# Performance work log

Measured on AMD Instinct MI355X. Metric: run time of the kernel, lower is better.

Reference implementation:

```python
import jax, jax.numpy as jnp
import numpy as np

B, T, H, W = 2, 32, 16, 16
D, NH = 256, 8
DH = D // NH


def _block_causal(Tn, block):
    # True = allowed to attend (block-lower-triangular over time blocks)
    base = jnp.triu(jnp.ones((Tn, Tn), bool), 1)
    return ~jnp.repeat(jnp.repeat(base, block, 0), block, 1)


def _ln(x, g, b, eps=1e-5):
    mu = x.mean(-1, keepdims=True)
    var = ((x - mu) ** 2).mean(-1, keepdims=True)
    return (x - mu) * jax.lax.rsqrt(var + eps) * g + b


def _attn(q, k, v, mask=None):
    # q,k,v: [Bf, S, h, dh]
    s = jnp.einsum('bqhd,bkhd->bhqk', q, k) * (q.shape[-1] ** -0.5)
    if mask is not None:
        s = jnp.where(mask, s, jnp.finfo(s.dtype).min)
    a = jax.nn.softmax(s, -1)
    return jnp.einsum('bhqk,bkhd->bqhd', a, v)


def setup_inputs() -> dict:
    key = jax.random.key(0)
    ks = iter(jax.random.split(key, 64))

    def lin(din, dout):
        return (jax.random.normal(next(ks), (din, dout), jnp.float32) * 0.02,
                jnp.zeros((dout,), jnp.float32))

    inp = {'x': jax.random.normal(next(ks), (B, T, H, W, D), jnp.float32)}
    inp['g1'] = jnp.ones((D,), jnp.float32); inp['b1'] = jnp.zeros((D,), jnp.float32)
    for plane in ('hw', 'ht', 'wt'):
        for p in ('q', 'k', 'v'):
            w, b = lin(D, D)
            inp[f'w{p}_{plane}'] = w
            inp[f'b{p}_{plane}'] = b
    inp['wo'], inp['bo'] = lin(D, D)
    inp['wg1'], inp['bg1'] = lin(D, D)
    inp['wg2'], inp['bg2'] = lin(D, 3 * NH)
    inp['g2'] = jnp.ones((D,), jnp.float32); inp['b2'] = jnp.zeros((D,), jnp.float32)
    inp['wm1'], inp['bm1'] = lin(D, 4 * D)
    inp['wm2'], inp['bm2'] = lin(4 * D, D)
    return inp


def reference(x, g1, b1,
              wq_hw, bq_hw, wk_hw, bk_hw, wv_hw, bv_hw,
              wq_ht, bq_ht, wk_ht, bk_ht, wv_ht, bv_ht,
              wq_wt, bq_wt, wk_wt, bk_wt, wv_wt, bv_wt,
              wo, bo, wg1, bg1, wg2, bg2, g2, b2,
              wm1, bm1, wm2, bm2):
    y = _ln(x, g1, b1)

    # HW plane: attention over H*W at each (B,T), non-causal
    def hw(w, b):
        return (y @ w + b).reshape(B * T, H * W, NH, DH)
    o_hw = _attn(hw(wq_hw, bq_hw), hw(wk_hw, bk_hw), hw(wv_hw, bv_hw))
    o_hw = o_hw.reshape(B, T, H, W, NH, DH)

    # HT plane: fixed W column, seq = T*H, block-causal in T (block H)
    def ht(w, b):
        return (y @ w + b).reshape(B, T, H, W, NH, DH).transpose(0, 3, 1, 2, 4, 5).reshape(B * W, T * H, NH, DH)
    mask_ht = _block_causal(T, H)[None, None]
    o_ht = _attn(ht(wq_ht, bq_ht), ht(wk_ht, bk_ht), ht(wv_ht, bv_ht), mask_ht)
    o_ht = o_ht.reshape(B, W, T, H, NH, DH).transpose(0, 2, 3, 1, 4, 5)

    # WT plane: fixed H row, seq = T*W, block-causal in T (block W)
    def wt(w, b):
        return (y @ w + b).reshape(B, T, H, W, NH, DH).transpose(0, 2, 1, 3, 4, 5).reshape(B * H, T * W, NH, DH)
    mask_wt = _block_causal(T, W)[None, None]
    o_wt = _attn(wt(wq_wt, bq_wt), wt(wk_wt, bk_wt), wt(wv_wt, bv_wt), mask_wt)
    o_wt = o_wt.reshape(B, H, T, W, NH, DH).transpose(0, 2, 1, 3, 4, 5)

    # per-head gated fusion across the three planes
    gates = jax.nn.softmax((jax.nn.silu(y @ wg1 + bg1) @ wg2 + bg2).reshape(B, T, H, W, NH, 3), -1)
    m = gates[..., 0:1] * o_hw + gates[..., 1:2] * o_ht + gates[..., 2:3] * o_wt

    x = x + m.reshape(B, T, H, W, D) @ wo + bo
    x = x + (jax.nn.gelu(_ln(x, g2, b2) @ wm1 + bm1, approximate=False) @ wm2 + bm2)
    return x
```

## Files before the change

### kernel.cpp

```cpp
#include <hip/hip_runtime.h>
#include <math.h>

#define NTOK 16384
#define DD   256
#define NHD  8
#define DHD  32

typedef unsigned short ushort_t;
using short8  = __attribute__((ext_vector_type(8))) short;
using floatx4 = __attribute__((ext_vector_type(4))) float;

__device__ __forceinline__ ushort_t f2bf(float f) {
  unsigned u = __float_as_uint(f);
  u = (u + 0x7FFFu + ((u >> 16) & 1u)) >> 16;
  return (ushort_t)u;
}

__device__ __forceinline__ float wave_sum(float v) {
#pragma unroll
  for (int off = 32; off; off >>= 1) v += __shfl_xor(v, off, 64);
  return v;
}

__global__ __launch_bounds__(256) void ln_bf_kernel(
    const float* __restrict__ x, const float* __restrict__ g,
    const float* __restrict__ b, ushort_t* __restrict__ y)
{
  const int row  = blockIdx.x * 4 + (threadIdx.x >> 6);
  const int lane = threadIdx.x & 63;
  const float4 xv = *(const float4*)&x[(size_t)row * DD + lane * 4];
  float s = xv.x + xv.y + xv.z + xv.w;
  s = wave_sum(s);
  const float mu = s * (1.0f / DD);
  const float dx = xv.x - mu, dy = xv.y - mu, dz = xv.z - mu, dw = xv.w - mu;
  float ss = dx * dx + dy * dy + dz * dz + dw * dw;
  ss = wave_sum(ss);
  const float rs = rsqrtf(ss * (1.0f / DD) + 1e-5f);
  const float4 gv = *(const float4*)&g[lane * 4];
  const float4 bv = *(const float4*)&b[lane * 4];
  ushort4 o;
  o.x = f2bf(dx * rs * gv.x + bv.x);
  o.y = f2bf(dy * rs * gv.y + bv.y);
  o.z = f2bf(dz * rs * gv.z + bv.z);
  o.w = f2bf(dw * rs * gv.w + bv.w);
  *(ushort4*)&y[(size_t)row * DD + lane * 4] = o;
}

struct W11 { const float* s[11]; ushort_t* d[11]; };

__global__ __launch_bounds__(256) void convw11_kernel(W11 p) {
  const int mi = blockIdx.y;
  const int idx = blockIdx.x * 256 + threadIdx.x;
  const int n = idx >> 8, k = idx & 255;
  p.d[mi][n * 256 + k] = f2bf(p.s[mi][k * 256 + n]);
}

template <int KK, int NN>
__global__ __launch_bounds__(256) void convw_kernel(
    const float* __restrict__ src, ushort_t* __restrict__ dst)
{
  const int idx = blockIdx.x * 256 + threadIdx.x;
  const int n = idx / KK, k = idx % KK;
  dst[n * KK + k] = f2bf(src[(size_t)k * NN + n]);
}

#define LDK 40

template <bool RES>
__device__ __forceinline__ void mgemm_body(
    const ushort_t* __restrict__ A, const ushort_t* __restrict__ Wt,
    const float* __restrict__ bias, const float* __restrict__ res,
    void* __restrict__ Cout, int M, int N, int K, int bx, int by,
    int act, bool obf)
{
  __shared__ ushort_t As[128 * LDK];
  __shared__ ushort_t Bs[128 * LDK];
  const int tid = threadIdx.x;
  const int wid = tid >> 6;
  const int lane = tid & 63;
  const int wm = (wid >> 1) * 64;
  const int wn = (wid & 1) * 64;
  const int m0 = by * 128, n0 = bx * 128;

  const int lrow = tid >> 1;
  const int lk   = (tid & 1) * 16;
  const int fr = lane & 15;
  const int fk = (lane >> 4) * 8;

  floatx4 acc[4][4] = {};

  uint4 av0 = *(const uint4*)&A[(size_t)(m0 + lrow) * K + lk];
  uint4 av1 = *(const uint4*)&A[(size_t)(m0 + lrow) * K + lk + 8];
  uint4 bv0 = *(const uint4*)&Wt[(size_t)(n0 + lrow) * K + lk];
  uint4 bv1 = *(const uint4*)&Wt[(size_t)(n0 + lrow) * K + lk + 8];

  for (int k0 = 0; k0 < K; k0 += 32) {
    __syncthreads();
    *(uint4*)&As[lrow * LDK + lk]     = av0;
    *(uint4*)&As[lrow * LDK + lk + 8] = av1;
    *(uint4*)&Bs[lrow * LDK + lk]     = bv0;
    *(uint4*)&Bs[lrow * LDK + lk + 8] = bv1;
    __syncthreads();
    if (k0 + 32 < K) {
      av0 = *(const uint4*)&A[(size_t)(m0 + lrow) * K + k0 + 32 + lk];
      av1 = *(const uint4*)&A[(size_t)(m0 + lrow) * K + k0 + 32 + lk + 8];
      bv0 = *(const uint4*)&Wt[(size_t)(n0 + lrow) * K + k0 + 32 + lk];
      bv1 = *(const uint4*)&Wt[(size_t)(n0 + lrow) * K + k0 + 32 + lk + 8];
    }
    short8 af[4], bf[4];
#pragma unroll
    for (int f = 0; f < 4; f++) {
      af[f] = *(const short8*)&As[(wm + f * 16 + fr) * LDK + fk];
      bf[f] = *(const short8*)&Bs[(wn + f * 16 + fr) * LDK + fk];
    }
#pragma unroll
    for (int i = 0; i < 4; i++)
#pragma unroll
      for (int j = 0; j < 4; j++)
        acc[i][j] = __builtin_amdgcn_mfma_f32_16x16x32_bf16(af[i], bf[j], acc[i][j], 0, 0, 0);
  }

  const int g4 = (lane >> 4) * 4;
#pragma unroll
  for (int i = 0; i < 4; i++) {
#pragma unroll
    for (int j = 0; j < 4; j++) {
      const int col = n0 + wn + j * 16 + fr;
      const float bb = bias[col];
#pragma unroll
      for (int r = 0; r < 4; r++) {
        const int row = m0 + wm + i * 16 + g4 + r;
        float v = acc[i][j][r] + bb;
        if (act == 1) v = v / (1.0f + __expf(-v));
        if (act == 2) v = 0.5f * v * (1.0f + erff(v * 0.70710678118654752f));
        if (RES) v += res[(size_t)row * N + col];
        if (obf) ((ushort_t*)Cout)[(size_t)row * N + col] = f2bf(v);
        else     ((float*)Cout)[(size_t)row * N + col] = v;
      }
    }
  }
}

template <int ACT, bool RES, bool OBF>
__global__ __launch_bounds__(256) void mgemm_kernel(
    const ushort_t* __restrict__ A, const ushort_t* __restrict__ Wt,
    const float* __restrict__ bias, const float* __restrict__ res,
    void* __restrict__ C, int M, int N, int K)
{
  mgemm_body<RES>(A, Wt, bias, res, C, M, N, K, blockIdx.x, blockIdx.y, ACT, OBF);
}

struct ProjArgs {
  const ushort_t* w[10];
  const float*    b[10];
  void*           c[10];
};

__global__ __launch_bounds__(256) void mgemm_proj_kernel(
    const ushort_t* __restrict__ A, ProjArgs p, int M, int N, int K)
{
  const int z = blockIdx.z;
  const int act = (z == 9) ? 1 : 0;
  const bool obf = (z != 9);
  mgemm_body<false>(A, p.w[z], p.b[z], nullptr, p.c[z], M, N, K,
                    blockIdx.x, blockIdx.y, act, obf);
}

template <bool RES>
__global__ __launch_bounds__(256) void mgemm64_kernel(
    const ushort_t* __restrict__ A, const ushort_t* __restrict__ Wt,
    const float* __restrict__ bias, const float* __restrict__ res,
    float* __restrict__ C, int M, int N, int K)
{
  __shared__ ushort_t As[64 * LDK];
  __shared__ ushort_t Bs[64 * LDK];
  const int tid = threadIdx.x;
  const int wid = tid >> 6;
  const int lane = tid & 63;
  const int wm = (wid >> 1) * 32;
  const int wn = (wid & 1) * 32;
  const int m0 = blockIdx.y * 64, n0 = blockIdx.x * 64;

  const int lr = tid >> 2;
  const int lq = (tid & 3) * 8;
  const int fr = lane & 15;
  const int fk = (lane >> 4) * 8;

  floatx4 acc[2][2] = {};

  uint4 av = *(const uint4*)&A[(size_t)(m0 + lr) * K + lq];
  uint4 bv = *(const uint4*)&Wt[(size_t)(n0 + lr) * K + lq];

  for (int k0 = 0; k0 < K; k0 += 32) {
    __syncthreads();
    *(uint4*)&As[lr * LDK + lq] = av;
    *(uint4*)&Bs[lr * LDK + lq] = bv;
    __syncthreads();
    if (k0 + 32 < K) {
      av = *(const uint4*)&A[(size_t)(m0 + lr) * K + k0 + 32 + lq];
      bv = *(const uint4*)&Wt[(size_t)(n0 + lr) * K + k0 + 32 + lq];
    }
    short8 af[2], bf[2];
#pragma unroll
    for (int f = 0; f < 2; f++) {
      af[f] = *(const short8*)&As[(wm + f * 16 + fr) * LDK + fk];
      bf[f] = *(const short8*)&Bs[(wn + f * 16 + fr) * LDK + fk];
    }
#pragma unroll
    for (int i = 0; i < 2; i++)
#pragma unroll
      for (int j = 0; j < 2; j++)
        acc[i][j] = __builtin_amdgcn_mfma_f32_16x16x32_bf16(af[i], bf[j], acc[i][j], 0, 0, 0);
  }

  const int g4 = (lane >> 4) * 4;
#pragma unroll
  for (int i = 0; i < 2; i++) {
#pragma unroll
    for (int j = 0; j < 2; j++) {
      const int col = n0 + wn + j * 16 + fr;
      const float bb = bias[col];
#pragma unroll
      for (int r = 0; r < 4; r++) {
        const int row = m0 + wm + i * 16 + g4 + r;
        float v = acc[i][j][r] + bb;
        if (RES) v += res[(size_t)row * N + col];
        C[(size_t)row * N + col] = v;
      }
    }
  }
}

__device__ __forceinline__ int tok_map_rt(int plane, int bb, int s) {
  if (plane == 0) return bb * 256 + s;
  if (plane == 1) return (bb >> 4) * 8192 + (s >> 4) * 256 + (s & 15) * 16 + (bb & 15);
  return (bb >> 4) * 8192 + (s >> 4) * 256 + (bb & 15) * 16 + (s & 15);
}

__global__ __launch_bounds__(256) void mattn_all_kernel(
    const ushort_t* __restrict__ qkv, float* __restrict__ ohw,
    float* __restrict__ oht, float* __restrict__ owt)
{
  __shared__ ushort_t Kls[64 * 40];
  __shared__ ushort_t Vt[32 * 72];
  __shared__ ushort_t Pls[4 * 16 * 72];

  const int head = blockIdx.x;
  const int yy = blockIdx.y;
  const int plane = yy >> 8;
  const int rm = yy & 255;
  int qc, bb, S;
  bool causal;
  if (plane == 0) { qc = rm >> 6; bb = rm & 63; S = 256; causal = false; }
  else            { qc = rm >> 5; bb = rm & 31; S = 512; causal = true;  }

  const size_t NDU = (size_t)NTOK * DD;
  const ushort_t* Qg = qkv + (size_t)(plane * 3 + 0) * NDU;
  const ushort_t* Kg = qkv + (size_t)(plane * 3 + 1) * NDU;
  const ushort_t* Vg = qkv + (size_t)(plane * 3 + 2) * NDU;
  float* Og = (plane == 0) ? ohw : (plane == 1) ? oht : owt;

  const int tid = threadIdx.x;
  const int wid = tid >> 6;
  const int lane = tid & 63;
  const int fr = lane & 15;
  const int hi = lane >> 4;
  const float scale = 0.17677669529663687f;

  const int q0 = qc * 64;

  const int qtok_a = tok_map_rt(plane, bb, q0 + wid * 16 + fr);
  const short8 qfrag = *(const short8*)&Qg[(size_t)qtok_a * DD + head * DHD + hi * 8];

  floatx4 o0 = {}, o1 = {};
  float mrun[4] = {-3e30f, -3e30f, -3e30f, -3e30f};
  float lrun[4] = {0.f, 0.f, 0.f, 0.f};

  const int lim = causal ? (q0 + wid * 16 + 16) : S;
  const int ntiles = (causal ? (q0 + 64) : S) >> 6;

  const int krow = tid >> 2;
  const int g    = tid & 3;
  const int kseg = g * 8;

  int ptok = tok_map_rt(plane, bb, krow);
  uint4 kv = *(const uint4*)&Kg[(size_t)ptok * DD + head * DHD + kseg];
  uint4 vv = *(const uint4*)&Vg[(size_t)ptok * DD + head * DHD + kseg];

  for (int t = 0; t < ntiles; t++) {
    __syncthreads();
    *(uint4*)&Kls[krow * 40 + kseg] = kv;
    {
      const ushort_t* vp = (const ushort_t*)&vv;
#pragma unroll
      for (int d = 0; d < 8; d++) {
        const int dim = kseg + d;
        Vt[dim * 72 + (((krow >> 3) ^ (dim >> 2)) << 3) + (krow & 7)] = vp[d];
      }
    }
    __syncthreads();
    if (t + 1 < ntiles) {
      ptok = tok_map_rt(plane, bb, (t + 1) * 64 + krow);
      kv = *(const uint4*)&Kg[(size_t)ptok * DD + head * DHD + kseg];
      vv = *(const uint4*)&Vg[(size_t)ptok * DD + head * DHD + kseg];
    }

    const int kt0 = t * 64;
    if (causal && kt0 >= lim) continue;
    const int kend = causal ? min(lim - kt0, 64) : 64;

    floatx4 sacc[4];
#pragma unroll
    for (int j = 0; j < 4; j++) {
      floatx4 z = {};
      const short8 kf = *(const short8*)&Kls[(j * 16 + fr) * 40 + hi * 8];
      sacc[j] = __builtin_amdgcn_mfma_f32_16x16x32_bf16(qfrag, kf, z, 0, 0, 0);
    }

    float sc[4][4];
    float mt[4] = {-3e30f, -3e30f, -3e30f, -3e30f};
#pragma unroll
    for (int j = 0; j < 4; j++) {
      const bool valid = !causal || (j * 16 + fr) < kend;
#pragma unroll
      for (int r = 0; r < 4; r++) {
        const float sv = valid ? sacc[j][r] * scale : -3e30f;
        sc[j][r] = sv;
        mt[r] = fmaxf(mt[r], sv);
      }
    }
#pragma unroll
    for (int r = 0; r < 4; r++) {
      mt[r] = fmaxf(mt[r], __shfl_xor(mt[r], 1, 64));
      mt[r] = fmaxf(mt[r], __shfl_xor(mt[r], 2, 64));
      mt[r] = fmaxf(mt[r], __shfl_xor(mt[r], 4, 64));
      mt[r] = fmaxf(mt[r], __shfl_xor(mt[r], 8, 64));
    }

    float corr[4], psum[4];
#pragma unroll
    for (int r = 0; r < 4; r++) {
      const float mnew = fmaxf(mrun[r], mt[r]);
      corr[r] = __expf(mrun[r] - mnew);
      mrun[r] = mnew;
      psum[r] = 0.f;
    }

    const int pbase = wid * (16 * 72);
#pragma unroll
    for (int j = 0; j < 4; j++) {
#pragma unroll
      for (int r = 0; r < 4; r++) {
        const float p = __expf(sc[j][r] - mrun[r]);
        const ushort_t pb = f2bf(p);
        psum[r] += __uint_as_float((unsigned)pb << 16);
        Pls[pbase + (hi * 4 + r) * 72 + (((2 * j + (fr >> 3)) ^ hi) << 3) + (fr & 7)] = pb;
      }
    }
#pragma unroll
    for (int r = 0; r < 4; r++) {
      psum[r] += __shfl_xor(psum[r], 1, 64);
      psum[r] += __shfl_xor(psum[r], 2, 64);
      psum[r] += __shfl_xor(psum[r], 4, 64);
      psum[r] += __shfl_xor(psum[r], 8, 64);
      lrun[r] = lrun[r] * corr[r] + psum[r];
      o0[r] *= corr[r];
      o1[r] *= corr[r];
    }

#pragma unroll
    for (int kh = 0; kh < 2; kh++) {
      const int bq = (hi + 4 * kh);
      const short8 pa  = *(const short8*)&Pls[pbase + fr * 72 + ((bq ^ (fr >> 2)) << 3)];
      const short8 vb0 = *(const short8*)&Vt[fr * 72 + ((bq ^ (fr >> 2)) << 3)];
      const short8 vb1 = *(const short8*)&Vt[(16 + fr) * 72 + ((bq ^ ((fr >> 2) + 4)) << 3)];
      o0 = __builtin_amdgcn_mfma_f32_16x16x32_bf16(pa, vb0, o0, 0, 0, 0);
      o1 = __builtin_amdgcn_mfma_f32_16x16x32_bf16(pa, vb1, o1, 0, 0, 0);
    }
  }

#pragma unroll
  for (int r = 0; r < 4; r++) {
    const float inv = 1.0f / lrun[r];
    const int otok = tok_map_rt(plane, bb, q0 + wid * 16 + hi * 4 + r);
    float* ob = &Og[(size_t)otok * DD + head * DHD];
    ob[fr] = o0[r] * inv;
    ob[16 + fr] = o1[r] * inv;
  }
}

__global__ __launch_bounds__(256) void gate_kernel(
    const float* __restrict__ t, const float* __restrict__ wg2,
    const float* __restrict__ bg2, float* __restrict__ gates)
{
  const int idx = blockIdx.x * 256 + threadIdx.x;
  const int token = idx >> 3, head = idx & 7;
  float a0 = bg2[head * 3 + 0], a1 = bg2[head * 3 + 1], a2 = bg2[head * 3 + 2];
  const float* trow = &t[(size_t)token * DD];
  const float* wbase = &wg2[head * 3];
  for (int k4 = 0; k4 < 64; k4++) {
    const float4 tv = *(const float4*)&trow[k4 * 4];
    const float* wr = &wbase[(k4 * 4) * 24];
    a0 = fmaf(tv.x, wr[0],      a0); a1 = fmaf(tv.x, wr[1],      a1); a2 = fmaf(tv.x, wr[2],      a2);
    a0 = fmaf(tv.y, wr[24 + 0], a0); a1 = fmaf(tv.y, wr[24 + 1], a1); a2 = fmaf(tv.y, wr[24 + 2], a2);
    a0 = fmaf(tv.z, wr[48 + 0], a0); a1 = fmaf(tv.z, wr[48 + 1], a1); a2 = fmaf(tv.z, wr[48 + 2], a2);
    a0 = fmaf(tv.w, wr[72 + 0], a0); a1 = fmaf(tv.w, wr[72 + 1], a1); a2 = fmaf(tv.w, wr[72 + 2], a2);
  }
  const float mx = fmaxf(a0, fmaxf(a1, a2));
  const float e0 = __expf(a0 - mx), e1 = __expf(a1 - mx), e2 = __expf(a2 - mx);
  const float inv = 1.0f / (e0 + e1 + e2);
  float* gp = &gates[(size_t)token * 24 + head * 3];
  gp[0] = e0 * inv; gp[1] = e1 * inv; gp[2] = e2 * inv;
}

__global__ __launch_bounds__(256) void combine_kernel(
    const float* __restrict__ gates, const float* __restrict__ ohw,
    const float* __restrict__ oht, const float* __restrict__ owt,
    ushort_t* __restrict__ m)
{
  const int idx = blockIdx.x * 256 + threadIdx.x;
  const int token = idx >> 6;
  const int head = (idx >> 3) & 7;
  const float* gp = &gates[(size_t)token * 24 + head * 3];
  const float g0 = gp[0], g1 = gp[1], g2 = gp[2];
  const float4 a = ((const float4*)ohw)[idx];
  const float4 b = ((const float4*)oht)[idx];
  const float4 c = ((const float4*)owt)[idx];
  ushort4 r;
  r.x = f2bf(g0 * a.x + g1 * b.x + g2 * c.x);
  r.y = f2bf(g0 * a.y + g1 * b.y + g2 * c.y);
  r.z = f2bf(g0 * a.z + g1 * b.z + g2 * c.z);
  r.w = f2bf(g0 * a.w + g1 * b.w + g2 * c.w);
  ((ushort4*)m)[idx] = r;
}

extern "C" void kernel_launch(void* const* d_in, const int* in_sizes, int n_in,
                              void* d_out, int out_size, void* d_ws, size_t ws_size,
                              hipStream_t stream)
{
  (void)in_sizes; (void)n_in; (void)out_size; (void)ws_size;
  const float* x   = (const float*)d_in[0];
  const float* g1  = (const float*)d_in[1];
  const float* b1  = (const float*)d_in[2];
  const float* wq[3] = {(const float*)d_in[3], (const float*)d_in[9],  (const float*)d_in[15]};
  const float* bq[3] = {(const float*)d_in[4], (const float*)d_in[10], (const float*)d_in[16]};
  const float* wk[3] = {(const float*)d_in[5], (const float*)d_in[11], (const float*)d_in[17]};
  const float* bk[3] = {(const float*)d_in[6], (const float*)d_in[12], (const float*)d_in[18]};
  const float* wv[3] = {(const float*)d_in[7], (const float*)d_in[13], (const float*)d_in[19]};
  const float* bv[3] = {(const float*)d_in[8], (const float*)d_in[14], (const float*)d_in[20]};
  const float* wo  = (const float*)d_in[21];
  const float* bo  = (const float*)d_in[22];
  const float* wg1 = (const float*)d_in[23];
  const float* bg1 = (const float*)d_in[24];
  const float* wg2 = (const float*)d_in[25];
  const float* bg2 = (const float*)d_in[26];
  const float* g2  = (const float*)d_in[27];
  const float* b2  = (const float*)d_in[28];
  const float* wm1 = (const float*)d_in[29];
  const float* bm1 = (const float*)d_in[30];
  const float* wm2 = (const float*)d_in[31];
  const float* bm2 = (const float*)d_in[32];

  const size_t NDU = (size_t)NTOK * DD;

  ushort_t* U = (ushort_t*)d_ws;
  ushort_t* Ybf  = U;
  ushort_t* Y2bf = U + NDU;
  ushort_t* qkvb = U + 2 * NDU;
  ushort_t* Mbf  = U + 11 * NDU;
  float* F   = (float*)(U + 12 * NDU);
  float* Ohw = F;
  float* Oht = Ohw + NDU;
  float* Owt = Oht + NDU;
  float* TX  = Owt + NDU;
  float* Gt  = TX + NDU;
  ushort_t* Wbf = (ushort_t*)(Gt + (size_t)NTOK * 24);
  ushort_t* wbf11[11];
  for (int i = 0; i < 11; i++) wbf11[i] = Wbf + (size_t)i * 65536;
  ushort_t* wm1bf = Wbf + (size_t)11 * 65536;
  ushort_t* wm2bf = wm1bf + 262144;
  ushort_t* Hh = qkvb;

  const dim3 blk(256);

  {
    W11 p;
    const float* srcs[11] = {wq[0], wk[0], wv[0], wq[1], wk[1], wv[1],
                             wq[2], wk[2], wv[2], wg1, wo};
    for (int i = 0; i < 11; i++) { p.s[i] = srcs[i]; p.d[i] = wbf11[i]; }
    convw11_kernel<<<dim3(256, 11), blk, 0, stream>>>(p);
    convw_kernel<256, 1024><<<1024, blk, 0, stream>>>(wm1, wm1bf);
    convw_kernel<1024, 256><<<1024, blk, 0, stream>>>(wm2, wm2bf);
  }

  ln_bf_kernel<<<NTOK / 4, blk, 0, stream>>>(x, g1, b1, Ybf);

  {
    ProjArgs p;
    for (int pl = 0; pl < 3; pl++) {
      p.w[pl * 3 + 0] = wbf11[pl * 3 + 0]; p.b[pl * 3 + 0] = bq[pl];
      p.w[pl * 3 + 1] = wbf11[pl * 3 + 1]; p.b[pl * 3 + 1] = bk[pl];
      p.w[pl * 3 + 2] = wbf11[pl * 3 + 2]; p.b[pl * 3 + 2] = bv[pl];
      for (int wch = 0; wch < 3; wch++)
        p.c[pl * 3 + wch] = qkvb + (size_t)(pl * 3 + wch) * NDU;
    }
    p.w[9] = wbf11[9]; p.b[9] = bg1; p.c[9] = TX;
    mgemm_proj_kernel<<<dim3(2, 128, 10), blk, 0, stream>>>(Ybf, p, NTOK, DD, DD);
  }

  gate_kernel<<<NTOK * NHD / 256, blk, 0, stream>>>(TX, wg2, bg2, Gt);

  mattn_all_kernel<<<dim3(NHD, 768), blk, 0, stream>>>(qkvb, Ohw, Oht, Owt);

  combine_kernel<<<NTOK * 64 / 256, blk, 0, stream>>>(Gt, Ohw, Oht, Owt, Mbf);

  mgemm64_kernel<true><<<dim3(4, 256), blk, 0, stream>>>(Mbf, wbf11[10], bo, x, TX, NTOK, DD, DD);

  ln_bf_kernel<<<NTOK / 4, blk, 0, stream>>>(TX, g2, b2, Y2bf);

  mgemm_kernel<2, false, true><<<dim3(8, 128), blk, 0, stream>>>(Y2bf, wm1bf, bm1, nullptr, Hh, NTOK, 1024, DD);

  mgemm64_kernel<true><<<dim3(4, 256), blk, 0, stream>>>(Hh, wm2bf, bm2, TX, (float*)d_out, NTOK, DD, 1024);
}
```

Baseline: 386.9 us.

## Fold attention scale into Q projection, transpose S, and tile weight conversion

The softmax scale is now applied in the Q-projection epilogue, so the attention kernel no longer multiplies each score. S is computed with K as the A operand, so each lane holds one query column. The row max and sum then need two cross-lane shuffles instead of four per row, and P is packed with v_cvt_pk_bf16_f32. Causal tiles skip the masked 16-key sub-blocks in both the QK and PV MFMAs. The three weight-conversion launches are merged into one LDS-tiled transpose kernel with coalesced reads and writes, which adds a broadcast shuffle for the correction and normalisation factors.

```diff
diff --git a/kernel.cpp b/kernel.cpp
--- a/kernel.cpp
+++ b/kernel.cpp
@@ -46,22 +46,29 @@
   *(ushort4*)&y[(size_t)row * DD + lane * 4] = o;
 }
 
-struct W11 { const float* s[11]; ushort_t* d[11]; };
-
-__global__ __launch_bounds__(256) void convw11_kernel(W11 p) {
-  const int mi = blockIdx.y;
-  const int idx = blockIdx.x * 256 + threadIdx.x;
-  const int n = idx >> 8, k = idx & 255;
-  p.d[mi][n * 256 + k] = f2bf(p.s[mi][k * 256 + n]);
-}
-
-template <int KK, int NN>
-__global__ __launch_bounds__(256) void convw_kernel(
-    const float* __restrict__ src, ushort_t* __restrict__ dst)
-{
-  const int idx = blockIdx.x * 256 + threadIdx.x;
-  const int n = idx / KK, k = idx % KK;
-  dst[n * KK + k] = f2bf(src[(size_t)k * NN + n]);
+struct TT { const float* s[19]; ushort_t* d[19]; int ss[19]; int ds[19]; };
+
+__global__ __launch_bounds__(256) void convt_kernel(TT p) {
+  __shared__ ushort_t t[64][65];
+  const int e = blockIdx.y;
+  const float* src = p.s[e];
+  ushort_t* dst = p.d[e];
+  const int ss = p.ss[e], ds = p.ds[e];
+  const int tr = (blockIdx.x & 3) * 64;
+  const int tc = (blockIdx.x >> 2) * 64;
+  const int lr = threadIdx.x >> 6;
+  const int lc = threadIdx.x & 63;
+#pragma unroll
+  for (int i = 0; i < 16; i++) {
+    const int r = i * 4 + lr;
+    t[r][lc] = f2bf(src[(size_t)(tr + r) * ss + tc + lc]);
+  }
+  __syncthreads();
+#pragma unroll
+  for (int i = 0; i < 16; i++) {
+    const int r = i * 4 + lr;
+    dst[(size_t)(tc + r) * ds + tr + lc] = t[lc][r];
+  }
 }
 
 #define LDK 40
@@ -71,7 +78,7 @@
     const ushort_t* __restrict__ A, const ushort_t* __restrict__ Wt,
     const float* __restrict__ bias, const float* __restrict__ res,
     void* __restrict__ Cout, int M, int N, int K, int bx, int by,
-    int act, bool obf)
+    int act, bool obf, float oscale)
 {
   __shared__ ushort_t As[128 * LDK];
   __shared__ ushort_t Bs[128 * LDK];
@@ -133,6 +140,7 @@
         float v = acc[i][j][r] + bb;
         if (act == 1) v = v / (1.0f + __expf(-v));
         if (act == 2) v = 0.5f * v * (1.0f + erff(v * 0.70710678118654752f));
+        v *= oscale;
         if (RES) v += res[(size_t)row * N + col];
         if (obf) ((ushort_t*)Cout)[(size_t)row * N + col] = f2bf(v);
         else     ((float*)Cout)[(size_t)row * N + col] = v;
@@ -147,7 +155,7 @@
     const float* __restrict__ bias, const float* __restrict__ res,
     void* __restrict__ C, int M, int N, int K)
 {
-  mgemm_body<RES>(A, Wt, bias, res, C, M, N, K, blockIdx.x, blockIdx.y, ACT, OBF);
+  mgemm_body<RES>(A, Wt, bias, res, C, M, N, K, blockIdx.x, blockIdx.y, ACT, OBF, 1.0f);
 }
 
 struct ProjArgs {
@@ -162,8 +170,9 @@
   const int z = blockIdx.z;
   const int act = (z == 9) ? 1 : 0;
   const bool obf = (z != 9);
+  const float osc = (z < 9 && (z % 3) == 0) ? 0.17677669529663687f : 1.0f;
   mgemm_body<false>(A, p.w[z], p.b[z], nullptr, p.c[z], M, N, K,
-                    blockIdx.x, blockIdx.y, act, obf);
+                    blockIdx.x, blockIdx.y, act, obf, osc);
 }
 
 template <bool RES>
@@ -243,7 +252,7 @@
 {
   __shared__ ushort_t Kls[64 * 40];
   __shared__ ushort_t Vt[32 * 72];
-  __shared__ ushort_t Pls[4 * 16 * 72];
+  __shared__ unsigned PlsU[4][16 * 36];
 
   const int head = blockIdx.x;
   const int yy = blockIdx.y;
@@ -265,7 +274,6 @@
   const int lane = tid & 63;
   const int fr = lane & 15;
   const int hi = lane >> 4;
-  const float scale = 0.17677669529663687f;
 
   const int q0 = qc * 64;
 
@@ -273,8 +281,7 @@
   const short8 qfrag = *(const short8*)&Qg[(size_t)qtok_a * DD + head * DHD + hi * 8];
 
   floatx4 o0 = {}, o1 = {};
-  float mrun[4] = {-3e30f, -3e30f, -3e30f, -3e30f};
-  float lrun[4] = {0.f, 0.f, 0.f, 0.f};
+  float mrun = -3e30f, lrun = 0.0f;
 
   const int lim = causal ? (q0 + wid * 16 + 16) : S;
   const int ntiles = (causal ? (q0 + 64) : S) >> 6;
@@ -307,85 +314,93 @@
 
     const int kt0 = t * 64;
     if (causal && kt0 >= lim) continue;
-    const int kend = causal ? min(lim - kt0, 64) : 64;
+    const int jend = causal ? (min(lim - kt0, 64) >> 4) : 4;
 
     floatx4 sacc[4];
 #pragma unroll
     for (int j = 0; j < 4; j++) {
-      floatx4 z = {};
-      const short8 kf = *(const short8*)&Kls[(j * 16 + fr) * 40 + hi * 8];
-      sacc[j] = __builtin_amdgcn_mfma_f32_16x16x32_bf16(qfrag, kf, z, 0, 0, 0);
-    }
-
-    float sc[4][4];
-    float mt[4] = {-3e30f, -3e30f, -3e30f, -3e30f};
+      if (j < jend) {
+        floatx4 z = {};
+        const short8 kf = *(const short8*)&Kls[(j * 16 + fr) * 40 + hi * 8];
+        sacc[j] = __builtin_amdgcn_mfma_f32_16x16x32_bf16(kf, qfrag, z, 0, 0, 0);
+      }
+    }
+
+    float mt = -3e30f;
 #pragma unroll
     for (int j = 0; j < 4; j++) {
-      const bool valid = !causal || (j * 16 + fr) < kend;
-#pragma unroll
-      for (int r = 0; r < 4; r++) {
-        const float sv = valid ? sacc[j][r] * scale : -3e30f;
-        sc[j][r] = sv;
-        mt[r] = fmaxf(mt[r], sv);
-      }
-    }
+      if (j < jend) {
+        const float m01 = fmaxf(sacc[j][0], sacc[j][1]);
+        const float m23 = fmaxf(sacc[j][2], sacc[j][3]);
+        mt = fmaxf(mt, fmaxf(m01, m23));
+      }
+    }
+    mt = fmaxf(mt, __shfl_xor(mt, 16, 64));
+    mt = fmaxf(mt, __shfl_xor(mt, 32, 64));
+
+    const float mnew = fmaxf(mrun, mt);
+    const float corr = __expf(mrun - mnew);
+    mrun = mnew;
+
+    float psum = 0.0f;
+    unsigned pk[8];
+#pragma unroll
+    for (int j = 0; j < 4; j++) {
+      if (j < jend) {
+        const float p0 = __expf(sacc[j][0] - mnew);
+        const float p1 = __expf(sacc[j][1] - mnew);
+        const float p2 = __expf(sacc[j][2] - mnew);
+        const float p3 = __expf(sacc[j][3] - mnew);
+        unsigned a, b;
+        asm("v_cvt_pk_bf16_f32 %0, %1, %2" : "=v"(a) : "v"(p0), "v"(p1));
+        asm("v_cvt_pk_bf16_f32 %0, %1, %2" : "=v"(b) : "v"(p2), "v"(p3));
+        pk[2 * j] = a; pk[2 * j + 1] = b;
+        psum += __uint_as_float(a << 16) + __uint_as_float(a & 0xFFFF0000u);
+        psum += __uint_as_float(b << 16) + __uint_as_float(b & 0xFFFF0000u);
+      } else {
+        pk[2 * j] = 0u; pk[2 * j + 1] = 0u;
+      }
+    }
+    psum += __shfl_xor(psum, 16, 64);
+    psum += __shfl_xor(psum, 32, 64);
+    lrun = lrun * corr + psum;
+
+    unsigned* prow = &PlsU[wid][fr * 36];
+#pragma unroll
+    for (int j = 0; j < 4; j++) {
+      prow[j * 8 + hi * 2]     = pk[2 * j];
+      prow[j * 8 + hi * 2 + 1] = pk[2 * j + 1];
+    }
+
 #pragma unroll
     for (int r = 0; r < 4; r++) {
-      mt[r] = fmaxf(mt[r], __shfl_xor(mt[r], 1, 64));
-      mt[r] = fmaxf(mt[r], __shfl_xor(mt[r], 2, 64));
-      mt[r] = fmaxf(mt[r], __shfl_xor(mt[r], 4, 64));
-      mt[r] = fmaxf(mt[r], __shfl_xor(mt[r], 8, 64));
-    }
-
-    float corr[4], psum[4];
-#pragma unroll
-    for (int r = 0; r < 4; r++) {
-      const float mnew = fmaxf(mrun[r], mt[r]);
-      corr[r] = __expf(mrun[r] - mnew);
-      mrun[r] = mnew;
-      psum[r] = 0.f;
-    }
-
-    const int pbase = wid * (16 * 72);
-#pragma unroll
-    for (int j = 0; j < 4; j++) {
-#pragma unroll
-      for (int r = 0; r < 4; r++) {
-        const float p = __expf(sc[j][r] - mrun[r]);
-        const ushort_t pb = f2bf(p);
-        psum[r] += __uint_as_float((unsigned)pb << 16);
-        Pls[pbase + (hi * 4 + r) * 72 + (((2 * j + (fr >> 3)) ^ hi) << 3) + (fr & 7)] = pb;
-      }
-    }
-#pragma unroll
-    for (int r = 0; r < 4; r++) {
-      psum[r] += __shfl_xor(psum[r], 1, 64);
-      psum[r] += __shfl_xor(psum[r], 2, 64);
-      psum[r] += __shfl_xor(psum[r], 4, 64);
-      psum[r] += __shfl_xor(psum[r], 8, 64);
-      lrun[r] = lrun[r] * corr[r] + psum[r];
-      o0[r] *= corr[r];
-      o1[r] *= corr[r];
-    }
-
+      const float cb = __shfl(corr, (lane & 48) + hi * 4 + r, 64);
+      o0[r] *= cb;
+      o1[r] *= cb;
+    }
+
+    const int khend = (jend > 2) ? 2 : 1;
 #pragma unroll
     for (int kh = 0; kh < 2; kh++) {
-      const int bq = (hi + 4 * kh);
-      const short8 pa  = *(const short8*)&Pls[pbase + fr * 72 + ((bq ^ (fr >> 2)) << 3)];
-      const short8 vb0 = *(const short8*)&Vt[fr * 72 + ((bq ^ (fr >> 2)) << 3)];
-      const short8 vb1 = *(const short8*)&Vt[(16 + fr) * 72 + ((bq ^ ((fr >> 2) + 4)) << 3)];
-      o0 = __builtin_amdgcn_mfma_f32_16x16x32_bf16(pa, vb0, o0, 0, 0, 0);
-      o1 = __builtin_amdgcn_mfma_f32_16x16x32_bf16(pa, vb1, o1, 0, 0, 0);
-    }
-  }
-
+      if (kh < khend) {
+        const short8 pa = *(const short8*)&PlsU[wid][fr * 36 + kh * 16 + hi * 4];
+        const int bq = hi + 4 * kh;
+        const short8 vb0 = *(const short8*)&Vt[fr * 72 + ((bq ^ (fr >> 2)) << 3)];
+        const short8 vb1 = *(const short8*)&Vt[(16 + fr) * 72 + ((bq ^ ((fr >> 2) + 4)) << 3)];
+        o0 = __builtin_amdgcn_mfma_f32_16x16x32_bf16(pa, vb0, o0, 0, 0, 0);
+        o1 = __builtin_amdgcn_mfma_f32_16x16x32_bf16(pa, vb1, o1, 0, 0, 0);
+      }
+    }
+  }
+
+  const float il0 = 1.0f / lrun;
 #pragma unroll
   for (int r = 0; r < 4; r++) {
-    const float inv = 1.0f / lrun[r];
+    const float il = __shfl(il0, (lane & 48) + hi * 4 + r, 64);
     const int otok = tok_map_rt(plane, bb, q0 + wid * 16 + hi * 4 + r);
     float* ob = &Og[(size_t)otok * DD + head * DHD];
-    ob[fr] = o0[r] * inv;
-    ob[16 + fr] = o1[r] * inv;
+    ob[fr] = o0[r] * il;
+    ob[16 + fr] = o1[r] * il;
   }
 }
 
@@ -484,13 +499,23 @@
   const dim3 blk(256);
 
   {
-    W11 p;
+    TT p;
     const float* srcs[11] = {wq[0], wk[0], wv[0], wq[1], wk[1], wv[1],
                              wq[2], wk[2], wv[2], wg1, wo};
-    for (int i = 0; i < 11; i++) { p.s[i] = srcs[i]; p.d[i] = wbf11[i]; }
-    convw11_kernel<<<dim3(256, 11), blk, 0, stream>>>(p);
-    convw_kernel<256, 1024><<<1024, blk, 0, stream>>>(wm1, wm1bf);
-    convw_kernel<1024, 256><<<1024, blk, 0, stream>>>(wm2, wm2bf);
+    for (int i = 0; i < 11; i++) {
+      p.s[i] = srcs[i]; p.d[i] = wbf11[i]; p.ss[i] = 256; p.ds[i] = 256;
+    }
+    for (int i = 0; i < 4; i++) {
+      p.s[11 + i] = wm1 + i * 256;
+      p.d[11 + i] = wm1bf + (size_t)(i * 256) * 256;
+      p.ss[11 + i] = 1024; p.ds[11 + i] = 256;
+    }
+    for (int i = 0; i < 4; i++) {
+      p.s[15 + i] = wm2 + (size_t)(i * 256) * 256;
+      p.d[15 + i] = wm2bf + i * 256;
+      p.ss[15 + i] = 256; p.ds[15 + i] = 1024;
+    }
+    convt_kernel<<<dim3(16, 19), blk, 0, stream>>>(p);
   }
 
   ln_bf_kernel<<<NTOK / 4, blk, 0, stream>>>(x, g1, b1, Ybf);
```

Measured after the change: 346.1 us. 10.5% less time.
